# Kernel optimization log

Hardware: AMD Instinct MI355X
Metric: run time of the kernel (lower is better)

The kernel has to match this reference:

```python
import jax, jax.numpy as jnp
import numpy as np

N, E, B = 4096, 12288, 64
CLIP, HID, H = 768, 1024, 4
PREFIX, MBART = 4, 768
C2 = PREFIX * MBART
NEG_SLOPE = 0.2


def setup_inputs() -> dict:
    key = jax.random.key(0)
    ks = jax.random.split(key, 30)
    s = 0.05

    def nrm(k, shape, sc=s):
        return jax.random.normal(k, shape, dtype=jnp.float32) * sc

    inp = {
        "x": nrm(ks[0], (N, CLIP), 1.0),
        "edge_index": jax.random.randint(ks[1], (2, E), 0, N),
        "edge_attr": nrm(ks[2], (E, CLIP), 1.0),
        "batch": jnp.sort(jax.random.randint(ks[3], (N,), 0, B)),
        # GATConv 1 (clip_dim -> hidden, H heads, concat=False)
        "W1": nrm(ks[4], (CLIP, H, HID)),
        "att_src1": nrm(ks[5], (H, HID)),
        "att_dst1": nrm(ks[6], (H, HID)),
        "W_edge1": nrm(ks[7], (CLIP, H, HID)),
        "att_edge1": nrm(ks[8], (H, HID)),
        "bias1": jnp.zeros((HID,), jnp.float32),
        "prelu1": jnp.float32(0.25),
        # GATConv 2 (hidden -> prefix*mbart, H heads, concat=False)
        "W2": nrm(ks[9], (HID, H, C2)),
        "att_src2": nrm(ks[10], (H, C2)),
        "att_dst2": nrm(ks[11], (H, C2)),
        "W_edge2": nrm(ks[12], (CLIP, H, C2)),
        "att_edge2": nrm(ks[13], (H, C2)),
        "bias2": jnp.zeros((C2,), jnp.float32),
        "prelu2": jnp.float32(0.25),
        # AttentionalAggregation gate_nn: Linear/PReLU/Linear/PReLU/Linear
        "gW1": nrm(ks[14], (C2, HID)),
        "gb1": jnp.zeros((HID,), jnp.float32),
        "ga1": jnp.float32(0.25),
        "gW2": nrm(ks[15], (HID, HID)),
        "gb2": jnp.zeros((HID,), jnp.float32),
        "ga2": jnp.float32(0.25),
        "gW3": nrm(ks[16], (HID, 1)),
        "gb3": jnp.zeros((1,), jnp.float32),
    }
    return inp


def _prelu(x, a):
    return jnp.where(x >= 0, x, a * x)


def _gat_conv(x, src, dst, edge_attr, W, att_s, att_d, W_e, att_e, bias, n):
    # PyG GATConv, concat=False: shared lin for src/dst, edge-attention term,
    # leaky_relu, segment softmax over destination neighborhoods, scatter-add.
    xl = jnp.einsum('nd,dhc->nhc', x, W)                  # [N,H,C]
    a_s = jnp.einsum('nhc,hc->nh', xl, att_s)             # [N,H]
    a_d = jnp.einsum('nhc,hc->nh', xl, att_d)             # [N,H]
    # fuse lin_edge + att_edge: alpha_e = edge_attr @ (W_e . att_e)
    w_e = jnp.einsum('dhc,hc->dh', W_e, att_e)            # [D_edge,H]
    a_e = edge_attr @ w_e                                 # [E,H]
    alpha = jax.nn.leaky_relu(a_s[src] + a_d[dst] + a_e, NEG_SLOPE)
    # segment softmax grouped by dst
    amax = jax.ops.segment_max(alpha, dst, num_segments=n)
    amax = jnp.where(jnp.isfinite(amax), amax, 0.0)
    ex = jnp.exp(alpha - amax[dst])
    den = jax.ops.segment_sum(ex, dst, num_segments=n)
    coef = ex / (den[dst] + 1e-16)                        # [E,H]
    msg = coef[:, :, None] * xl[src]                      # [E,H,C]
    out = jax.ops.segment_sum(msg, dst, num_segments=n)   # [N,H,C]
    return out.mean(axis=1) + bias                        # concat=False -> head mean


def _forward(x, edge_index, edge_attr, batch,
             W1, att_src1, att_dst1, W_edge1, att_edge1, bias1, prelu1,
             W2, att_src2, att_dst2, W_edge2, att_edge2, bias2, prelu2,
             gW1, gb1, ga1, gW2, gb2, ga2, gW3, gb3):
    n = x.shape[0]
    src, dst = edge_index[0], edge_index[1]
    # add_self_loops with fill_value='mean': self-loop edge_attr = mean of
    # incoming edge_attr per destination node (0 if isolated)
    ones = jnp.ones((src.shape[0],), x.dtype)
    deg = jax.ops.segment_sum(ones, dst, num_segments=n)
    mean_attr = jax.ops.segment_sum(edge_attr, dst, num_segments=n) / jnp.clip(deg, 1.0)[:, None]
    loops = jnp.arange(n)
    src_a = jnp.concatenate([src, loops])
    dst_a = jnp.concatenate([dst, loops])
    ea = jnp.concatenate([edge_attr, mean_attr], axis=0)

    h = _gat_conv(x, src_a, dst_a, ea, W1, att_src1, att_dst1, W_edge1, att_edge1, bias1, n)
    h = _prelu(h, prelu1)
    h = _gat_conv(h, src_a, dst_a, ea, W2, att_src2, att_dst2, W_edge2, att_edge2, bias2, n)
    h = _prelu(h, prelu2)

    # AttentionalAggregation: gate_nn -> segment softmax over batch -> weighted sum
    g = _prelu(h @ gW1 + gb1, ga1)
    g = _prelu(g @ gW2 + gb2, ga2)
    gate = g @ gW3 + gb3                                   # [N,1]
    gmax = jax.ops.segment_max(gate, batch, num_segments=B)
    gmax = jnp.where(jnp.isfinite(gmax), gmax, 0.0)
    eg = jnp.exp(gate - gmax[batch])
    den = jax.ops.segment_sum(eg, batch, num_segments=B)
    coef = eg / (den[batch] + 1e-16)
    pooled = jax.ops.segment_sum(coef * h, batch, num_segments=B)  # [B,C2]
    return pooled.reshape(-1, PREFIX, MBART)


def reference(x, edge_index, edge_attr, batch,
              W1, att_src1, att_dst1, W_edge1, att_edge1, bias1, prelu1,
              W2, att_src2, att_dst2, W_edge2, att_edge2, bias2, prelu2,
              gW1, gb1, ga1, gW2, gb2, ga2, gW3, gb3):
    return _forward(x, edge_index, edge_attr, batch,
                    W1, att_src1, att_dst1, W_edge1, att_edge1, bias1, prelu1,
                    W2, att_src2, att_dst2, W_edge2, att_edge2, bias2, prelu2,
                    gW1, gb1, ga1, gW2, gb2, ga2, gW3, gb3)
```

## Files before the change

kernel.cpp:

```cpp
#include <hip/hip_runtime.h>
#include <stdint.h>
#include <stddef.h>

#define N_NODES  4096
#define N_EDGES  12288
#define EA_EDGES 16384
#define NBATCH   64
#define CLIPD    768
#define HIDD     1024
#define C2D      3072
#define NEG_SLOPE 0.2f
#define MAXDEG   96

typedef unsigned short u16;
typedef short bf16x8 __attribute__((ext_vector_type(8)));
typedef float f32x4  __attribute__((ext_vector_type(4)));

static __device__ __forceinline__ float b2f(u16 u) {
    union { float f; unsigned int i; } v; v.i = ((unsigned int)u) << 16; return v.f;
}
static __device__ __forceinline__ u16 f2b(float f) {
    union { float f; unsigned int i; } v; v.f = f;
    unsigned int r = (v.i + 0x7fffu + ((v.i >> 16) & 1u)) >> 16;
    return (u16)r;
}
static __device__ __forceinline__ void ld4(const float* p, float v[4]) {
    float4 t = *(const float4*)p;
    v[0] = t.x; v[1] = t.y; v[2] = t.z; v[3] = t.w;
}
static __device__ __forceinline__ void ld4(const u16* p, float v[4]) {
    ushort4 t = *(const ushort4*)p;
    v[0] = b2f(t.x); v[1] = b2f(t.y); v[2] = b2f(t.z); v[3] = b2f(t.w);
}

static __device__ __forceinline__ float wsum(float v) {
#pragma unroll
    for (int o = 32; o > 0; o >>= 1) v += __shfl_xor(v, o, 64);
    return v;
}
static __device__ __forceinline__ float wmax(float v) {
#pragma unroll
    for (int o = 32; o > 0; o >>= 1) v = fmaxf(v, __shfl_xor(v, o, 64));
    return v;
}
static __device__ __forceinline__ int lower_bound(const int* a, int n, int key) {
    int lo = 0, hi = n;
    while (lo < hi) { int m = (lo + hi) >> 1; if (a[m] < key) lo = m + 1; else hi = m; }
    return lo;
}

#define GLD16(gp, lp)                                                            \
    __builtin_amdgcn_global_load_lds((const __attribute__((address_space(1))) void*)(gp), \
                                     (__attribute__((address_space(3))) void*)(lp), 16, 0, 0)

__global__ void k_deg(const int* __restrict__ dst, int* __restrict__ deg) {
    int e = blockIdx.x * 256 + threadIdx.x;
    if (e < N_EDGES) atomicAdd(&deg[dst[e]], 1);
}

__global__ void k_scan(const int* __restrict__ deg, int* __restrict__ offs) {
    __shared__ int s[1024];
    int t = threadIdx.x;
    int v[4]; int sum = 0;
#pragma unroll
    for (int i = 0; i < 4; i++) { v[i] = deg[t * 4 + i] + 1; sum += v[i]; }
    s[t] = sum; __syncthreads();
    for (int st = 1; st < 1024; st <<= 1) {
        int x = 0;
        if (t >= st) x = s[t - st];
        __syncthreads();
        s[t] += x;
        __syncthreads();
    }
    int run = s[t] - sum;
#pragma unroll
    for (int i = 0; i < 4; i++) { offs[t * 4 + i] = run; run += v[i]; }
    if (t == 1023) offs[N_NODES] = run;
}

__global__ void k_fill(const int* __restrict__ dst, const int* __restrict__ offs,
                       int* __restrict__ cur, int* __restrict__ csr) {
    int id = blockIdx.x * 256 + threadIdx.x;
    if (id >= EA_EDGES) return;
    int d = (id < N_EDGES) ? dst[id] : (id - N_EDGES);
    int p = atomicAdd(&cur[d], 1);
    csr[offs[d] + p] = id;
}

static __device__ void reduce_w_body(const float* __restrict__ W, const float* __restrict__ attA,
                                     const float* __restrict__ attB, float* __restrict__ out,
                                     int C, int col0, int d) {
    int t = threadIdx.x;
    float acc[8] = {0, 0, 0, 0, 0, 0, 0, 0};
    for (int c = t * 4; c < C; c += 1024) {
#pragma unroll
        for (int h = 0; h < 4; h++) {
            float4 w = *(const float4*)&W[((size_t)d * 4 + h) * C + c];
            float4 a = *(const float4*)&attA[h * C + c];
            acc[h] += w.x * a.x + w.y * a.y + w.z * a.z + w.w * a.w;
            if (attB) {
                float4 bv = *(const float4*)&attB[h * C + c];
                acc[4 + h] += w.x * bv.x + w.y * bv.y + w.z * bv.z + w.w * bv.w;
            }
        }
    }
    __shared__ float red[4][8];
    int lane = t & 63, wv = t >> 6;
#pragma unroll
    for (int j = 0; j < 8; j++) acc[j] = wsum(acc[j]);
    if (lane == 0) {
#pragma unroll
        for (int j = 0; j < 8; j++) red[wv][j] = acc[j];
    }
    __syncthreads();
    if (t < 8) {
        float s = red[0][t] + red[1][t] + red[2][t] + red[3][t];
        if (attB) out[d * 8 + col0 + t] = s;
        else if (t < 4) out[d * 8 + col0 + t] = s;
    }
}

__global__ void k_reduce_all(const float* __restrict__ W1, const float* __restrict__ as1,
                             const float* __restrict__ ad1, float* __restrict__ vsd1,
                             const float* __restrict__ We1, const float* __restrict__ ae1,
                             const float* __restrict__ W2, const float* __restrict__ as2,
                             const float* __restrict__ ad2, float* __restrict__ vsd2,
                             const float* __restrict__ We2, const float* __restrict__ ae2,
                             float* __restrict__ we12) {
    int b = blockIdx.x;
    if (b < CLIPD)                   reduce_w_body(W1, as1, ad1, vsd1, HIDD, 0, b);
    else if (b < 2 * CLIPD)          reduce_w_body(We1, ae1, nullptr, we12, HIDD, 0, b - CLIPD);
    else if (b < 2 * CLIPD + HIDD)   reduce_w_body(W2, as2, ad2, vsd2, C2D, 0, b - 2 * CLIPD);
    else                             reduce_w_body(We2, ae2, nullptr, we12, C2D, 4, b - 2 * CLIPD - HIDD);
}

template <typename T>
static __device__ void gemv8_body(const T* __restrict__ X, int K, const float* __restrict__ Wr,
                                  float* __restrict__ out, int row) {
    int lane = threadIdx.x & 63;
    float acc[8] = {0, 0, 0, 0, 0, 0, 0, 0};
    const T* xp = X + (size_t)row * K;
    for (int k = lane * 4; k < K; k += 256) {
        float xv[4]; ld4(xp + k, xv);
#pragma unroll
        for (int kk = 0; kk < 4; kk++) {
            const float4* w = (const float4*)(Wr + (size_t)(k + kk) * 8);
            float4 w0 = w[0], w1 = w[1];
            acc[0] += xv[kk] * w0.x; acc[1] += xv[kk] * w0.y;
            acc[2] += xv[kk] * w0.z; acc[3] += xv[kk] * w0.w;
            acc[4] += xv[kk] * w1.x; acc[5] += xv[kk] * w1.y;
            acc[6] += xv[kk] * w1.z; acc[7] += xv[kk] * w1.w;
        }
    }
#pragma unroll
    for (int j = 0; j < 8; j++) acc[j] = wsum(acc[j]);
    if (lane == 0) {
#pragma unroll
        for (int j = 0; j < 8; j++) out[(size_t)row * 8 + j] = acc[j];
    }
}

template <typename T>
__global__ void k_gemv8(const T* __restrict__ X, int K, const float* __restrict__ Wr,
                        float* __restrict__ out, int rows) {
    int row = blockIdx.x * 4 + (threadIdx.x >> 6);
    if (row < rows) gemv8_body(X, K, Wr, out, row);
}

__global__ void k_gemv8_dual(const float* __restrict__ Xa, const float* __restrict__ Wa,
                             float* __restrict__ outA, int rowsA,
                             const float* __restrict__ Xb, const float* __restrict__ Wb,
                             float* __restrict__ outB) {
    int row = blockIdx.x * 4 + (threadIdx.x >> 6);
    if (row < rowsA) gemv8_body(Xa, CLIPD, Wa, outA, row);
    else             gemv8_body(Xb, CLIPD, Wb, outB, row - rowsA);
}

template <typename T>
__global__ void k_attn_agg(const T* __restrict__ feat, int D,
                           const float* __restrict__ asd, const float* __restrict__ ae, int aecol,
                           const int* __restrict__ offs, const int* __restrict__ csr,
                           const int* __restrict__ src, u16* __restrict__ agg) {
    int n = blockIdx.x, t = threadIdx.x;
    __shared__ int sl[MAXDEG];
    __shared__ float cf[MAXDEG][4];
    __shared__ float er[MAXDEG][4];
    __shared__ int sidx;
    if (t == 0) sidx = -1;
    int lo = offs[n];
    int cnt = offs[n + 1] - lo;
    if (cnt > MAXDEG) cnt = MAXDEG;
    __syncthreads();
    for (int i = t; i < cnt; i += 256) {
        int eid = csr[lo + i];
        bool slf = (eid >= N_EDGES);
        int s = slf ? n : src[eid];
        sl[i] = s;
        if (slf) sidx = i;
#pragma unroll
        for (int h = 0; h < 4; h++) {
            float aev = slf ? 0.f : ae[(size_t)eid * 8 + aecol + h];
            er[i][h] = aev;
            float al = asd[(size_t)s * 8 + h] + asd[(size_t)n * 8 + 4 + h] + aev;
            cf[i][h] = (al >= 0.f) ? al : NEG_SLOPE * al;
        }
    }
    __syncthreads();
    int wv = t >> 6, lane = t & 63;
    {
        float se = 0.f;
        for (int i = lane; i < cnt; i += 64) se += er[i][wv];
        se = wsum(se);
        if (lane == 0 && sidx >= 0) {
            float al = asd[(size_t)n * 8 + wv] + asd[(size_t)n * 8 + 4 + wv] +
                       se / (float)(cnt > 1 ? cnt - 1 : 1);
            cf[sidx][wv] = (al >= 0.f) ? al : NEG_SLOPE * al;
        }
    }
    __syncthreads();
    {
        float mx = -1e30f;
        for (int i = lane; i < cnt; i += 64) mx = fmaxf(mx, cf[i][wv]);
        mx = wmax(mx);
        float ds = 0.f;
        for (int i = lane; i < cnt; i += 64) {
            float e = __expf(cf[i][wv] - mx); cf[i][wv] = e; ds += e;
        }
        ds = wsum(ds);
        float inv = 1.0f / (ds + 1e-16f);
        for (int i = lane; i < cnt; i += 64) cf[i][wv] *= inv;
    }
    __syncthreads();
    for (int d4 = t * 4; d4 < D; d4 += 1024) {
        float a[4][4] = {};
        for (int i = 0; i < cnt; i++) {
            float4 c4 = *(const float4*)cf[i];
            float v[4]; ld4(feat + (size_t)sl[i] * D + d4, v);
#pragma unroll
            for (int dj = 0; dj < 4; dj++) {
                a[dj][0] += c4.x * v[dj]; a[dj][1] += c4.y * v[dj];
                a[dj][2] += c4.z * v[dj]; a[dj][3] += c4.w * v[dj];
            }
        }
        u16* op = agg + (size_t)n * 4 * D + (size_t)d4 * 4;
#pragma unroll
        for (int dj = 0; dj < 4; dj++) {
            ushort4 pk;
            pk.x = f2b(a[dj][0]); pk.y = f2b(a[dj][1]);
            pk.z = f2b(a[dj][2]); pk.w = f2b(a[dj][3]);
            *(ushort4*)(op + dj * 4) = pk;
        }
    }
}

static __device__ void transpose_body(const float* __restrict__ in, u16* __restrict__ out,
                                      int R, int C, int bx, int by) {
    __shared__ float tile[64][65];
    int tx = threadIdx.x, ty = threadIdx.y;
    int rb = by * 64, cb = bx * 64;
    for (int i = ty; i < 64; i += 4) tile[i][tx] = in[(size_t)(rb + i) * C + cb + tx];
    __syncthreads();
    int linear = ty * 64 + tx;
#pragma unroll
    for (int jj = 0; jj < 4; jj++) {
        int idx = linear + jj * 256;
        int j = idx >> 4, s4 = (idx & 15) * 4;
        ushort4 pk;
        pk.x = f2b(tile[s4 + 0][j]);
        pk.y = f2b(tile[s4 + 1][j]);
        pk.z = f2b(tile[s4 + 2][j]);
        pk.w = f2b(tile[s4 + 3][j]);
        *(ushort4*)(out + (size_t)(cb + j) * R + rb + s4) = pk;
    }
}

__global__ void k_transpose(const float* __restrict__ in, u16* __restrict__ out, int R, int C) {
    transpose_body(in, out, R, C, blockIdx.x, blockIdx.y);
}

__global__ void k_transpose_all(const float* __restrict__ W1, u16* __restrict__ W1t,
                                const float* __restrict__ W2, u16* __restrict__ W2t,
                                const float* __restrict__ gW1, u16* __restrict__ gW1t,
                                const float* __restrict__ gW2, u16* __restrict__ gW2t) {
    int b = blockIdx.x;
    const float* in; u16* out; int R, C, lb, txc;
    if (b < 768)       { in = W1;  out = W1t;  R = 3072; C = 1024; lb = b;        txc = 16; }
    else if (b < 3840) { in = W2;  out = W2t;  R = 4096; C = 3072; lb = b - 768;  txc = 48; }
    else if (b < 4608) { in = gW1; out = gW1t; R = 3072; C = 1024; lb = b - 3840; txc = 16; }
    else               { in = gW2; out = gW2t; R = 1024; C = 1024; lb = b - 4608; txc = 16; }
    transpose_body(in, out, R, C, lb % txc, lb / txc);
}

template <int BN, int KSUB, int GATE>
static __device__ __forceinline__ void gemm_body(
        const u16* __restrict__ A, const u16* __restrict__ Bt, void* __restrict__ Cout,
        const float* __restrict__ bias, const float* __restrict__ prelu, float scale,
        int N, int K, int f32out,
        const float* __restrict__ gW3, float* __restrict__ gateOut) {
    constexpr int NJ = BN / 32;
    constexpr int NBCH = BN * 8 / 256;
    __shared__ __align__(16) u16 As[KSUB * 128 * 64];
    __shared__ __align__(16) u16 Bs[KSUB * BN * 64];
    int tid = threadIdx.x;
    int lane = tid & 63, wv = tid >> 6;
    int gx = gridDim.x;
    int bx = blockIdx.x, by = blockIdx.y;
    if ((gx & 7) == 0) {
        int flat = by * gx + bx;
        int nx_per = gx >> 3;
        int xcd = flat & 7, idx = flat >> 3;
        bx = xcd * nx_per + idx % nx_per;
        by = idx / nx_per;
    }
    int m0 = by * 128, n0 = bx * BN;
    const u16* agp[4]; int alo[4];
#pragma unroll
    for (int u = 0; u < 4; u++) {
        int c = tid + u * 256;
        int r = c >> 3, kb = (c & 7) ^ (r & 7);
        agp[u] = A + (size_t)(m0 + r) * K + kb * 8;
        alo[u] = c * 8;
    }
    const u16* bgp[NBCH]; int blo[NBCH];
#pragma unroll
    for (int u = 0; u < NBCH; u++) {
        int c = tid + u * 256;
        int r = c >> 3, kb = (c & 7) ^ (r & 7);
        bgp[u] = Bt + (size_t)(n0 + r) * K + kb * 8;
        blo[u] = c * 8;
    }
    int wm = wv & 1, wn = wv >> 1;
    int rl = lane & 15, q = lane >> 4;
    int swz = rl & 7;
    int mb = wm * 64 + rl;
    int nb = wn * (NJ * 16) + rl;
    f32x4 acc[4][NJ] = {};
    for (int k0 = 0; k0 < K; k0 += 64 * KSUB) {
        __syncthreads();
#pragma unroll
        for (int su = 0; su < KSUB; su++) {
#pragma unroll
            for (int u = 0; u < 4; u++)    GLD16(agp[u] + su * 64, As + su * (128 * 64) + alo[u]);
#pragma unroll
            for (int u = 0; u < NBCH; u++) GLD16(bgp[u] + su * 64, Bs + su * (BN * 64) + blo[u]);
        }
#pragma unroll
        for (int u = 0; u < 4; u++)    agp[u] += 64 * KSUB;
#pragma unroll
        for (int u = 0; u < NBCH; u++) bgp[u] += 64 * KSUB;
        __syncthreads();
#pragma unroll
        for (int su = 0; su < KSUB; su++) {
            const u16* Asb = As + su * (128 * 64);
            const u16* Bsb = Bs + su * (BN * 64);
            bf16x8 af[4][2];
#pragma unroll
            for (int i = 0; i < 4; i++)
#pragma unroll
                for (int s = 0; s < 2; s++)
                    af[i][s] = *(const bf16x8*)(Asb + (((mb + i * 16) * 8 + ((q + 4 * s) ^ swz)) * 8));
#pragma unroll
            for (int j = 0; j < NJ; j++) {
                bf16x8 b0 = *(const bf16x8*)(Bsb + (((nb + j * 16) * 8 + ((q + 4 * 0) ^ swz)) * 8));
                bf16x8 b1 = *(const bf16x8*)(Bsb + (((nb + j * 16) * 8 + ((q + 4 * 1) ^ swz)) * 8));
#pragma unroll
                for (int i = 0; i < 4; i++) {
                    acc[i][j] = __builtin_amdgcn_mfma_f32_16x16x32_bf16(af[i][0], b0, acc[i][j], 0, 0, 0);
                    acc[i][j] = __builtin_amdgcn_mfma_f32_16x16x32_bf16(af[i][1], b1, acc[i][j], 0, 0, 0);
                }
            }
        }
    }
    float pa = prelu[0];
    int r0w = (lane >> 4) * 4;
    int cc = lane & 15;
    if (GATE) {
        float w3[NJ], bvj[NJ];
#pragma unroll
        for (int j = 0; j < NJ; j++) {
            int col = n0 + wn * (NJ * 16) + j * 16 + cc;
            w3[j] = gW3[col];
            bvj[j] = bias[col];
        }
#pragma unroll
        for (int i = 0; i < 4; i++) {
#pragma unroll
            for (int r = 0; r < 4; r++) {
                float p = 0.f;
#pragma unroll
                for (int j = 0; j < NJ; j++) {
                    float v = acc[i][j][r] * scale + bvj[j];
                    v = (v >= 0.f) ? v : pa * v;
                    p += v * w3[j];
                }
                p += __shfl_xor(p, 1, 64); p += __shfl_xor(p, 2, 64);
                p += __shfl_xor(p, 4, 64); p += __shfl_xor(p, 8, 64);
                if (cc == 0) {
                    int row = m0 + wm * 64 + i * 16 + r0w + r;
                    atomicAdd(&gateOut[row], p);
                }
            }
        }
        return;
    }
#pragma unroll
    for (int j = 0; j < NJ; j++) {
        int col = n0 + wn * (NJ * 16) + j * 16 + cc;
        float bv = bias[col];
#pragma unroll
        for (int i = 0; i < 4; i++) {
#pragma unroll
            for (int r = 0; r < 4; r++) {
                int row = m0 + wm * 64 + i * 16 + r0w + r;
                float v = acc[i][j][r] * scale + bv;
                v = (v >= 0.f) ? v : pa * v;
                if (f32out) ((float*)Cout)[(size_t)row * N + col] = v;
                else        ((u16*)Cout)[(size_t)row * N + col] = f2b(v);
            }
        }
    }
}

__global__ __launch_bounds__(256, 2) void k_gemm_big(
        const u16* __restrict__ A, const u16* __restrict__ Bt, void* __restrict__ Cout,
        const float* __restrict__ bias, const float* __restrict__ prelu, float scale,
        int N, int K) {
    gemm_body<256, 1, 0>(A, Bt, Cout, bias, prelu, scale, N, K, 0, nullptr, nullptr);
}
__global__ __launch_bounds__(256, 2) void k_gemm_l1(
        const u16* __restrict__ A, const u16* __restrict__ Bt, void* __restrict__ Cout,
        const float* __restrict__ bias, const float* __restrict__ prelu, float scale,
        int N, int K) {
    gemm_body<64, 2, 0>(A, Bt, Cout, bias, prelu, scale, N, K, 0, nullptr, nullptr);
}
__global__ __launch_bounds__(256, 2) void k_gemm_g1(
        const u16* __restrict__ A, const u16* __restrict__ Bt, void* __restrict__ Cout,
        const float* __restrict__ bias, const float* __restrict__ prelu, float scale,
        int N, int K) {
    gemm_body<64, 2, 0>(A, Bt, Cout, bias, prelu, scale, N, K, 0, nullptr, nullptr);
}
__global__ __launch_bounds__(256, 2) void k_gemm_g2(
        const u16* __restrict__ A, const u16* __restrict__ Bt,
        const float* __restrict__ bias, const float* __restrict__ prelu,
        int N, int K, const float* __restrict__ gW3, float* __restrict__ gateOut) {
    gemm_body<64, 2, 1>(A, Bt, nullptr, bias, prelu, 1.0f, N, K, 0, gW3, gateOut);
}

__global__ void k_pool(const float* __restrict__ gate, const u16* __restrict__ h2,
                       const int* __restrict__ batch, float* __restrict__ out) {
    int b = blockIdx.x, t = threadIdx.x;
    int c = blockIdx.y * 1024 + t * 4;
    int lo = lower_bound(batch, N_NODES, b);
    int hi = lower_bound(batch, N_NODES, b + 1);
    int cnt = hi - lo;
    if (cnt <= 0) {
        float4 z; z.x = z.y = z.z = z.w = 0.f;
        *(float4*)(out + (size_t)b * C2D + c) = z;
        return;
    }
    if (cnt > 256) cnt = 256;
    __shared__ float w[256];
    __shared__ float red[4];
    int lane = t & 63, wv = t >> 6;
    float mx = -1e30f;
    for (int i = t; i < cnt; i += 256) mx = fmaxf(mx, gate[lo + i]);
    mx = wmax(mx);
    if (lane == 0) red[wv] = mx;
    __syncthreads();
    mx = fmaxf(fmaxf(red[0], red[1]), fmaxf(red[2], red[3]));
    __syncthreads();
    float ds = 0.f;
    for (int i = t; i < cnt; i += 256) { float e = __expf(gate[lo + i] - mx); w[i] = e; ds += e; }
    ds = wsum(ds);
    if (lane == 0) red[wv] = ds;
    __syncthreads();
    float inv = 1.0f / (red[0] + red[1] + red[2] + red[3] + 1e-16f);
    float4 acc; acc.x = acc.y = acc.z = acc.w = 0.f;
    const u16* hp = h2 + (size_t)lo * C2D + c;
    for (int i = 0; i < cnt; i++) {
        ushort4 hv = *(const ushort4*)hp; hp += C2D;
        float wi = w[i];
        acc.x += wi * b2f(hv.x); acc.y += wi * b2f(hv.y);
        acc.z += wi * b2f(hv.z); acc.w += wi * b2f(hv.w);
    }
    acc.x *= inv; acc.y *= inv; acc.z *= inv; acc.w *= inv;
    *(float4*)(out + (size_t)b * C2D + c) = acc;
}

extern "C" void kernel_launch(void* const* d_in, const int* in_sizes, int n_in,
                              void* d_out, int out_size, void* d_ws, size_t ws_size,
                              hipStream_t stream) {
    (void)in_sizes; (void)n_in; (void)out_size;
    const float* x      = (const float*)d_in[0];
    const int*   eidx   = (const int*)d_in[1];
    const float* eattr  = (const float*)d_in[2];
    const int*   batch  = (const int*)d_in[3];
    const float* W1     = (const float*)d_in[4];
    const float* att_s1 = (const float*)d_in[5];
    const float* att_d1 = (const float*)d_in[6];
    const float* We1    = (const float*)d_in[7];
    const float* att_e1 = (const float*)d_in[8];
    const float* bias1  = (const float*)d_in[9];
    const float* prelu1 = (const float*)d_in[10];
    const float* W2     = (const float*)d_in[11];
    const float* att_s2 = (const float*)d_in[12];
    const float* att_d2 = (const float*)d_in[13];
    const float* We2    = (const float*)d_in[14];
    const float* att_e2 = (const float*)d_in[15];
    const float* bias2  = (const float*)d_in[16];
    const float* prelu2 = (const float*)d_in[17];
    const float* gW1    = (const float*)d_in[18];
    const float* gb1    = (const float*)d_in[19];
    const float* ga1    = (const float*)d_in[20];
    const float* gW2    = (const float*)d_in[21];
    const float* gb2    = (const float*)d_in[22];
    const float* ga2    = (const float*)d_in[23];
    const float* gW3    = (const float*)d_in[24];
    const int* srcA = eidx;
    const int* dstA = eidx + N_EDGES;

    char* wp = (char*)d_ws;
    auto alloc = [&](size_t bytes) -> void* {
        void* p = (void*)wp; wp += (bytes + 255) & ~(size_t)255; return p;
    };
    int*   deg  = (int*)alloc(N_NODES * 4);
    int*   cur  = (int*)alloc(N_NODES * 4);
    int*   offs = (int*)alloc((N_NODES + 1) * 4);
    int*   csr  = (int*)alloc(EA_EDGES * 4);
    float* vsd1 = (float*)alloc(CLIPD * 8 * 4);
    float* we12 = (float*)alloc(CLIPD * 8 * 4);
    float* vsd2 = (float*)alloc(HIDD * 8 * 4);
    float* ae   = (float*)alloc((size_t)N_EDGES * 8 * 4);
    float* asd1 = (float*)alloc((size_t)N_NODES * 8 * 4);
    float* asd2 = (float*)alloc((size_t)N_NODES * 8 * 4);
    float* gate = (float*)alloc(N_NODES * 4);
    char*  aggU = (char*)alloc((size_t)N_NODES * 4096 * 2);
    u16*   agg1 = (u16*)aggU;
    u16*   agg2 = (u16*)aggU;
    u16*   h1   = (u16*)alloc((size_t)N_NODES * HIDD * 2);
    u16*   g1   = h1;
    u16*   h2   = (u16*)alloc((size_t)N_NODES * C2D * 2);
    size_t used = (size_t)(wp - (char*)d_ws);
    bool fused_tr = (ws_size == 0) || (ws_size > used + (size_t)42 * 1024 * 1024);
    u16 *W1t, *W2t, *gW1t, *gW2t;
    if (fused_tr) {
        W1t  = (u16*)alloc((size_t)1024 * 3072 * 2);
        W2t  = (u16*)alloc((size_t)3072 * 4096 * 2);
        gW1t = (u16*)alloc((size_t)1024 * 3072 * 2);
        gW2t = (u16*)alloc((size_t)1024 * 1024 * 2);
    } else {
        u16* Btb = (u16*)alloc((size_t)C2D * 4096 * 2);
        W1t = W2t = gW1t = gW2t = Btb;
    }

    hipMemsetAsync(deg, 0, N_NODES * 4, stream);
    hipMemsetAsync(cur, 0, N_NODES * 4, stream);
    hipMemsetAsync(gate, 0, N_NODES * 4, stream);

    k_deg<<<(N_EDGES + 255) / 256, 256, 0, stream>>>(dstA, deg);
    k_scan<<<1, 1024, 0, stream>>>(deg, offs);
    k_fill<<<(EA_EDGES + 255) / 256, 256, 0, stream>>>(dstA, offs, cur, csr);

    k_reduce_all<<<2 * CLIPD + HIDD + CLIPD, 256, 0, stream>>>(
        W1, att_s1, att_d1, vsd1, We1, att_e1, W2, att_s2, att_d2, vsd2, We2, att_e2, we12);
    if (fused_tr)
        k_transpose_all<<<4864, dim3(64, 4), 0, stream>>>(W1, W1t, W2, W2t, gW1, gW1t, gW2, gW2t);

    k_gemv8_dual<<<(N_EDGES + N_NODES) / 4, 256, 0, stream>>>(
        eattr, we12, ae, N_EDGES, x, vsd1, asd1);

    k_attn_agg<float><<<N_NODES, 256, 0, stream>>>(x, CLIPD, asd1, ae, 0, offs, csr, srcA, agg1);
    if (!fused_tr)
        k_transpose<<<dim3(HIDD / 64, C2D / 64), dim3(64, 4), 0, stream>>>(W1, W1t, C2D, HIDD);
    k_gemm_l1<<<dim3(HIDD / 64, N_NODES / 128), 256, 0, stream>>>(
        agg1, W1t, h1, bias1, prelu1, 0.25f, HIDD, C2D);

    k_gemv8<u16><<<N_NODES / 4, 256, 0, stream>>>(h1, HIDD, vsd2, asd2, N_NODES);
    k_attn_agg<u16><<<N_NODES, 256, 0, stream>>>(h1, HIDD, asd2, ae, 4, offs, csr, srcA, agg2);
    if (!fused_tr)
        k_transpose<<<dim3(C2D / 64, 4096 / 64), dim3(64, 4), 0, stream>>>(W2, W2t, 4096, C2D);
    k_gemm_big<<<dim3(C2D / 256, N_NODES / 128), 256, 0, stream>>>(
        agg2, W2t, h2, bias2, prelu2, 0.25f, C2D, 4096);

    if (!fused_tr)
        k_transpose<<<dim3(HIDD / 64, C2D / 64), dim3(64, 4), 0, stream>>>(gW1, gW1t, C2D, HIDD);
    k_gemm_g1<<<dim3(HIDD / 64, N_NODES / 128), 256, 0, stream>>>(
        h2, gW1t, g1, gb1, ga1, 1.0f, HIDD, C2D);
    if (!fused_tr)
        k_transpose<<<dim3(HIDD / 64, HIDD / 64), dim3(64, 4), 0, stream>>>(gW2, gW2t, HIDD, HIDD);
    k_gemm_g2<<<dim3(HIDD / 64, N_NODES / 128), 256, 0, stream>>>(
        g1, gW2t, gb2, ga2, HIDD, HIDD, gW3, gate);

    k_pool<<<dim3(NBATCH, 3), 256, 0, stream>>>(gate, h2, batch, (float*)d_out);
}
```

Baseline: 556.9 us.

## Fuse attention-vector reduction into weight transpose and shrink big GEMM tile

The W1/W2 attention projections (vsd) are now computed inside the fused transpose kernel while each weight tile is loaded. Each block does wave reductions and atomics into zeroed vsd buffers, so the separate reduce pass no longer re-reads W1 and W2. The GEMM inner loop now preloads all B fragments before issuing MFMAs. The big GEMM tile width drops from 256 to 128 to double the block count. The atomics add contention and make the summation order nondeterministic, and the smaller tile reduces per-block data reuse.

```diff
diff --git a/kernel.cpp b/kernel.cpp
--- a/kernel.cpp
+++ b/kernel.cpp
@@ -132,6 +132,14 @@
     else if (b < 2 * CLIPD)          reduce_w_body(We1, ae1, nullptr, we12, HIDD, 0, b - CLIPD);
     else if (b < 2 * CLIPD + HIDD)   reduce_w_body(W2, as2, ad2, vsd2, C2D, 0, b - 2 * CLIPD);
     else                             reduce_w_body(We2, ae2, nullptr, we12, C2D, 4, b - 2 * CLIPD - HIDD);
+}
+
+__global__ void k_reduce_we(const float* __restrict__ We1, const float* __restrict__ ae1,
+                            const float* __restrict__ We2, const float* __restrict__ ae2,
+                            float* __restrict__ we12) {
+    int b = blockIdx.x;
+    if (b < CLIPD) reduce_w_body(We1, ae1, nullptr, we12, HIDD, 0, b);
+    else           reduce_w_body(We2, ae2, nullptr, we12, C2D, 4, b - CLIPD);
 }
 
 template <typename T>
@@ -254,11 +262,36 @@
 }
 
 static __device__ void transpose_body(const float* __restrict__ in, u16* __restrict__ out,
-                                      int R, int C, int bx, int by) {
+                                      int R, int C, int bx, int by,
+                                      const float* __restrict__ attS,
+                                      const float* __restrict__ attD,
+                                      float* __restrict__ vsd) {
     __shared__ float tile[64][65];
     int tx = threadIdx.x, ty = threadIdx.y;
     int rb = by * 64, cb = bx * 64;
-    for (int i = ty; i < 64; i += 4) tile[i][tx] = in[(size_t)(rb + i) * C + cb + tx];
+    float as_[4], ad_[4];
+    if (attS) {
+#pragma unroll
+        for (int h = 0; h < 4; h++) {
+            as_[h] = attS[h * C + cb + tx];
+            ad_[h] = attD[h * C + cb + tx];
+        }
+    }
+    for (int i = ty; i < 64; i += 4) {
+        float v = in[(size_t)(rb + i) * C + cb + tx];
+        tile[i][tx] = v;
+        if (attS) {
+            int r = rb + i;
+            int h = r & 3;
+            float ps = wsum(v * as_[h]);
+            float pd = wsum(v * ad_[h]);
+            if (tx == 0) {
+                int d = r >> 2;
+                atomicAdd(&vsd[d * 8 + h], ps);
+                atomicAdd(&vsd[d * 8 + 4 + h], pd);
+            }
+        }
+    }
     __syncthreads();
     int linear = ty * 64 + tx;
 #pragma unroll
@@ -275,20 +308,29 @@
 }
 
 __global__ void k_transpose(const float* __restrict__ in, u16* __restrict__ out, int R, int C) {
-    transpose_body(in, out, R, C, blockIdx.x, blockIdx.y);
-}
-
-__global__ void k_transpose_all(const float* __restrict__ W1, u16* __restrict__ W1t,
-                                const float* __restrict__ W2, u16* __restrict__ W2t,
-                                const float* __restrict__ gW1, u16* __restrict__ gW1t,
-                                const float* __restrict__ gW2, u16* __restrict__ gW2t) {
+    transpose_body(in, out, R, C, blockIdx.x, blockIdx.y, nullptr, nullptr, nullptr);
+}
+
+__global__ void k_transpose_red_all(
+        const float* __restrict__ W1, u16* __restrict__ W1t,
+        const float* __restrict__ as1, const float* __restrict__ ad1, float* __restrict__ vsd1,
+        const float* __restrict__ W2, u16* __restrict__ W2t,
+        const float* __restrict__ as2, const float* __restrict__ ad2, float* __restrict__ vsd2,
+        const float* __restrict__ gW1, u16* __restrict__ gW1t,
+        const float* __restrict__ gW2, u16* __restrict__ gW2t) {
     int b = blockIdx.x;
-    const float* in; u16* out; int R, C, lb, txc;
-    if (b < 768)       { in = W1;  out = W1t;  R = 3072; C = 1024; lb = b;        txc = 16; }
-    else if (b < 3840) { in = W2;  out = W2t;  R = 4096; C = 3072; lb = b - 768;  txc = 48; }
-    else if (b < 4608) { in = gW1; out = gW1t; R = 3072; C = 1024; lb = b - 3840; txc = 16; }
-    else               { in = gW2; out = gW2t; R = 1024; C = 1024; lb = b - 4608; txc = 16; }
-    transpose_body(in, out, R, C, lb % txc, lb / txc);
+    if (b < 768) {
+        transpose_body(W1, W1t, 3072, 1024, b % 16, b / 16, as1, ad1, vsd1);
+    } else if (b < 3840) {
+        int lb = b - 768;
+        transpose_body(W2, W2t, 4096, 3072, lb % 48, lb / 48, as2, ad2, vsd2);
+    } else if (b < 4608) {
+        int lb = b - 3840;
+        transpose_body(gW1, gW1t, 3072, 1024, lb % 16, lb / 16, nullptr, nullptr, nullptr);
+    } else {
+        int lb = b - 4608;
+        transpose_body(gW2, gW2t, 1024, 1024, lb % 16, lb / 16, nullptr, nullptr, nullptr);
+    }
 }
 
 template <int BN, int KSUB, int GATE>
@@ -353,22 +395,24 @@
         for (int su = 0; su < KSUB; su++) {
             const u16* Asb = As + su * (128 * 64);
             const u16* Bsb = Bs + su * (BN * 64);
-            bf16x8 af[4][2];
+            bf16x8 af[4][2], bfr[NJ][2];
 #pragma unroll
             for (int i = 0; i < 4; i++)
 #pragma unroll
                 for (int s = 0; s < 2; s++)
                     af[i][s] = *(const bf16x8*)(Asb + (((mb + i * 16) * 8 + ((q + 4 * s) ^ swz)) * 8));
 #pragma unroll
-            for (int j = 0; j < NJ; j++) {
-                bf16x8 b0 = *(const bf16x8*)(Bsb + (((nb + j * 16) * 8 + ((q + 4 * 0) ^ swz)) * 8));
-                bf16x8 b1 = *(const bf16x8*)(Bsb + (((nb + j * 16) * 8 + ((q + 4 * 1) ^ swz)) * 8));
-#pragma unroll
-                for (int i = 0; i < 4; i++) {
-                    acc[i][j] = __builtin_amdgcn_mfma_f32_16x16x32_bf16(af[i][0], b0, acc[i][j], 0, 0, 0);
-                    acc[i][j] = __builtin_amdgcn_mfma_f32_16x16x32_bf16(af[i][1], b1, acc[i][j], 0, 0, 0);
+            for (int j = 0; j < NJ; j++)
+#pragma unroll
+                for (int s = 0; s < 2; s++)
+                    bfr[j][s] = *(const bf16x8*)(Bsb + (((nb + j * 16) * 8 + ((q + 4 * s) ^ swz)) * 8));
+#pragma unroll
+            for (int i = 0; i < 4; i++)
+#pragma unroll
+                for (int j = 0; j < NJ; j++) {
+                    acc[i][j] = __builtin_amdgcn_mfma_f32_16x16x32_bf16(af[i][0], bfr[j][0], acc[i][j], 0, 0, 0);
+                    acc[i][j] = __builtin_amdgcn_mfma_f32_16x16x32_bf16(af[i][1], bfr[j][1], acc[i][j], 0, 0, 0);
                 }
-            }
         }
     }
     float pa = prelu[0];
@@ -425,7 +469,7 @@
         const u16* __restrict__ A, const u16* __restrict__ Bt, void* __restrict__ Cout,
         const float* __restrict__ bias, const float* __restrict__ prelu, float scale,
         int N, int K) {
-    gemm_body<256, 1, 0>(A, Bt, Cout, bias, prelu, scale, N, K, 0, nullptr, nullptr);
+    gemm_body<128, 1, 0>(A, Bt, Cout, bias, prelu, scale, N, K, 0, nullptr, nullptr);
 }
 __global__ __launch_bounds__(256, 2) void k_gemm_l1(
         const u16* __restrict__ A, const u16* __restrict__ Bt, void* __restrict__ Cout,
@@ -556,15 +600,24 @@
     hipMemsetAsync(deg, 0, N_NODES * 4, stream);
     hipMemsetAsync(cur, 0, N_NODES * 4, stream);
     hipMemsetAsync(gate, 0, N_NODES * 4, stream);
+    if (fused_tr) {
+        hipMemsetAsync(vsd1, 0, CLIPD * 8 * 4, stream);
+        hipMemsetAsync(vsd2, 0, HIDD * 8 * 4, stream);
+    }
 
     k_deg<<<(N_EDGES + 255) / 256, 256, 0, stream>>>(dstA, deg);
     k_scan<<<1, 1024, 0, stream>>>(deg, offs);
     k_fill<<<(EA_EDGES + 255) / 256, 256, 0, stream>>>(dstA, offs, cur, csr);
 
-    k_reduce_all<<<2 * CLIPD + HIDD + CLIPD, 256, 0, stream>>>(
-        W1, att_s1, att_d1, vsd1, We1, att_e1, W2, att_s2, att_d2, vsd2, We2, att_e2, we12);
-    if (fused_tr)
-        k_transpose_all<<<4864, dim3(64, 4), 0, stream>>>(W1, W1t, W2, W2t, gW1, gW1t, gW2, gW2t);
+    if (fused_tr) {
+        k_reduce_we<<<2 * CLIPD, 256, 0, stream>>>(We1, att_e1, We2, att_e2, we12);
+        k_transpose_red_all<<<4864, dim3(64, 4), 0, stream>>>(
+            W1, W1t, att_s1, att_d1, vsd1, W2, W2t, att_s2, att_d2, vsd2,
+            gW1, gW1t, gW2, gW2t);
+    } else {
+        k_reduce_all<<<2 * CLIPD + HIDD + CLIPD, 256, 0, stream>>>(
+            W1, att_s1, att_d1, vsd1, We1, att_e1, W2, att_s2, att_d2, vsd2, We2, att_e2, we12);
+    }
 
     k_gemv8_dual<<<(N_EDGES + N_NODES) / 4, 256, 0, stream>>>(
         eattr, we12, ae, N_EDGES, x, vsd1, asd1);
@@ -579,7 +632,7 @@
     k_attn_agg<u16><<<N_NODES, 256, 0, stream>>>(h1, HIDD, asd2, ae, 4, offs, csr, srcA, agg2);
     if (!fused_tr)
         k_transpose<<<dim3(C2D / 64, 4096 / 64), dim3(64, 4), 0, stream>>>(W2, W2t, 4096, C2D);
-    k_gemm_big<<<dim3(C2D / 256, N_NODES / 128), 256, 0, stream>>>(
+    k_gemm_big<<<dim3(C2D / 128, N_NODES / 128), 256, 0, stream>>>(
         agg2, W2t, h2, bias2, prelu2, 0.25f, C2D, 4096);
 
     if (!fused_tr)
```

New measurement: 607.1 us. +9.0%, slower.
